# Kernel tuning notes

Measured on AMD Instinct MI355X. Metric: run time of the kernel, lower is better.

The kernel has to match this reference:

```python
import jax, jax.numpy as jnp
import numpy as np

C_FEAT = 512
HID = 256
OUT = 3
IN_DIM = C_FEAT + 2 + 2  # feat + rel_coord + rel_cell = 516


def _nearest_idx(g, size):
    # grid_sample nearest, align_corners=False: unnormalize then round (half-to-even)
    x = ((g + 1.0) * size - 1.0) / 2.0
    return jnp.clip(jnp.round(x).astype(jnp.int32), 0, size - 1)


def setup_inputs() -> dict:
    key = jax.random.key(0)
    ks = jax.random.split(key, 12)
    B, Q, H, W = 2, 65536, 48, 48
    feat = jax.random.normal(ks[0], (B, C_FEAT, H, W), dtype=jnp.float32)
    coord = jax.random.uniform(ks[1], (B, Q, 2), dtype=jnp.float32, minval=-1.0, maxval=1.0)
    cell = jnp.full((B, Q, 2), 2.0 / 256.0, dtype=jnp.float32)  # query at 256x256 output res
    def lin_init(k, fan_in, fan_out):
        s = 1.0 / np.sqrt(fan_in)
        return jax.random.uniform(k, (fan_in, fan_out), jnp.float32, -s, s)
    W0 = lin_init(ks[2], IN_DIM, HID); b0 = jnp.zeros((HID,), jnp.float32)
    W1 = lin_init(ks[3], HID, HID);    b1 = jnp.zeros((HID,), jnp.float32)
    W2 = lin_init(ks[4], HID, HID);    b2 = jnp.zeros((HID,), jnp.float32)
    W3 = lin_init(ks[5], HID, HID);    b3 = jnp.zeros((HID,), jnp.float32)
    W4 = lin_init(ks[6], HID, OUT);    b4 = jnp.zeros((OUT,), jnp.float32)
    return {"feat": feat, "coord": coord, "cell": cell,
            "W0": W0, "b0": b0, "W1": W1, "b1": b1, "W2": W2, "b2": b2,
            "W3": W3, "b3": b3, "W4": W4, "b4": b4}


def _liif(feat, coord, cell, W0, b0, W1, b1, W2, b2, W3, b3, W4, b4):
    B, C, H, W = feat.shape
    Q = coord.shape[1]
    rx = 1.0 / H  # 2 / H / 2
    ry = 1.0 / W
    eps = 1e-6
    # local ensemble shifts (vx, vy) in order [(-1,-1),(-1,1),(1,-1),(1,1)]
    shifts = jnp.array([[-1., -1.], [-1., 1.], [1., -1.], [1., 1.]], dtype=feat.dtype)
    off = shifts * jnp.array([rx, ry], dtype=feat.dtype) + eps  # [4,2]
    coord_s = jnp.clip(coord[None] + off[:, None, None, :], -1 + 1e-6, 1 - 1e-6)  # [4,B,Q,2]
    # coord[...,0] indexes H (rows), coord[...,1] indexes W (cols) [code flips before grid_sample]
    idx_r = _nearest_idx(coord_s[..., 0], H)  # [4,B,Q]
    idx_c = _nearest_idx(coord_s[..., 1], W)
    lin = idx_r * W + idx_c                   # [4,B,Q]
    flat = feat.reshape(B, C, H * W).transpose(0, 2, 1)  # [B,HW,C]
    q_feat = jnp.take_along_axis(flat[None], lin[..., None], axis=2)  # [4,B,Q,C]
    # feat_coord grid_sample == center coord of the gathered cell
    qc_r = (idx_r.astype(feat.dtype) + 0.5) * (2.0 / H) - 1.0
    qc_c = (idx_c.astype(feat.dtype) + 0.5) * (2.0 / W) - 1.0
    rel = jnp.stack([(coord[None, ..., 0] - qc_r) * H,
                     (coord[None, ..., 1] - qc_c) * W], axis=-1)  # [4,B,Q,2]
    rel_cell = cell * jnp.array([H, W], dtype=feat.dtype)          # [B,Q,2]
    rel_cell4 = jnp.broadcast_to(rel_cell[None], (4, B, Q, 2))
    inp = jnp.concatenate([q_feat, rel, rel_cell4], axis=-1)       # [4,B,Q,516]
    # shared per-point MLP
    h = jax.nn.relu(inp @ W0 + b0)
    h = jax.nn.relu(h @ W1 + b1)
    h = jax.nn.relu(h @ W2 + b2)
    h = jax.nn.relu(h @ W3 + b3)
    pred = h @ W4 + b4                                             # [4,B,Q,3]
    area = jnp.abs(rel[..., 0] * rel[..., 1]) + 1e-9               # [4,B,Q]
    tot = area.sum(axis=0)
    # swap areas 0<->3 and 1<->2 (diagonal weighting) == reverse
    w = area[::-1] / tot[None]
    return (pred * w[..., None]).sum(axis=0)                       # [B,Q,3]


def reference(feat, coord, cell, W0, b0, W1, b1, W2, b2, W3, b3, W4, b4):
    return _liif(feat, coord, cell, W0, b0, W1, b1, W2, b2, W3, b3, W4, b4)
```

## Files before the change

kernel.cpp:

```cpp
#include <hip/hip_runtime.h>
#include <hip/hip_bf16.h>
#include <math.h>

#define HH    48
#define CFEAT 512
#define HID   256
#define NPOS  (HH*HH)
#define TQ    32
#define NEV   128

typedef __attribute__((ext_vector_type(8))) short bf16x8;
typedef __attribute__((ext_vector_type(4))) float f32x4;

static __device__ __forceinline__ unsigned short f2bf(float x) {
  unsigned int u = __float_as_uint(x);
  u += 0x7fffu + ((u >> 16) & 1u);
  return (unsigned short)(u >> 16);
}

static __device__ __forceinline__ unsigned int pk2bf(float a, float b) {
  __hip_bfloat162 h2 = __float22bfloat162_rn(make_float2(a, b));
  unsigned int u; __builtin_memcpy(&u, &h2, 4); return u;
}

static __device__ __forceinline__ void rel_calc(float c0, float c1, int s,
                                                float& r0, float& r1,
                                                int& ir, int& ic) {
  float vx = (s & 2) ? 1.0f : -1.0f;
  float vy = (s & 1) ? 1.0f : -1.0f;
  const float RXY = (float)(1.0/48.0);
  const float CLO = (float)(-1.0 + 1e-6);
  const float CHI = (float)( 1.0 - 1e-6);
  float gx = __fadd_rn(c0, __fadd_rn(__fmul_rn(vx, RXY), 1e-6f));
  float gy = __fadd_rn(c1, __fadd_rn(__fmul_rn(vy, RXY), 1e-6f));
  gx = fminf(fmaxf(gx, CLO), CHI);
  gy = fminf(fmaxf(gy, CLO), CHI);
  float xr = __fmul_rn(__fsub_rn(__fmul_rn(__fadd_rn(gx, 1.0f), 48.0f), 1.0f), 0.5f);
  float xc = __fmul_rn(__fsub_rn(__fmul_rn(__fadd_rn(gy, 1.0f), 48.0f), 1.0f), 0.5f);
  ir = (int)rintf(xr); ir = ir < 0 ? 0 : (ir > HH-1 ? HH-1 : ir);
  ic = (int)rintf(xc); ic = ic < 0 ? 0 : (ic > HH-1 ? HH-1 : ic);
  const float T2 = (float)(2.0/48.0);
  float qcr = __fsub_rn(__fmul_rn(__fadd_rn((float)ir, 0.5f), T2), 1.0f);
  float qcc = __fsub_rn(__fmul_rn(__fadd_rn((float)ic, 0.5f), T2), 1.0f);
  r0 = __fmul_rn(__fsub_rn(c0, qcr), 48.0f);
  r1 = __fmul_rn(__fsub_rn(c1, qcc), 48.0f);
}

__global__ __launch_bounds__(256) void liif_precompute(
    const float* __restrict__ feat, const float* __restrict__ W0,
    const float* __restrict__ b0, float* __restrict__ P)
{
  int blk = blockIdx.x;
  int b   = blk / (NPOS/4);
  int p0  = (blk - b*(NPOS/4)) * 4;
  int n   = threadIdx.x;
  const float* f = feat + (size_t)b * CFEAT * NPOS + p0;
  float bias = b0[n];
  float a0 = bias, a1 = bias, a2 = bias, a3 = bias;
  #pragma unroll 4
  for (int c = 0; c < CFEAT; ++c) {
    float w = W0[c*HID + n];
    const float* fr = f + (size_t)c * NPOS;
    a0 += fr[0]*w; a1 += fr[1]*w; a2 += fr[2]*w; a3 += fr[3]*w;
  }
  float* Pp = P + ((size_t)b*NPOS + p0)*HID + n;
  Pp[0*HID] = a0; Pp[1*HID] = a1; Pp[2*HID] = a2; Pp[3*HID] = a3;
}

__global__ __launch_bounds__(256) void liif_convert(
    const float* __restrict__ W1, const float* __restrict__ W2,
    const float* __restrict__ W3, const float* __restrict__ W4,
    unsigned char* __restrict__ img, float* __restrict__ w4t)
{
  int blk = blockIdx.x, t = threadIdx.x;
  if (blk < 24) {
    int l = blk >> 3, kc = blk & 7;
    const float* W = (l == 0) ? W1 : (l == 1) ? W2 : W3;
    unsigned short* dst = (unsigned short*)(img + (size_t)blk * 16384);
    #pragma unroll 1
    for (int s = 0; s < 4; ++s) {
      int p    = t + s*256;
      int wc   = p >> 8;
      int nt   = (p >> 6) & 3;
      int lane = p & 63;
      int lr   = lane & 15, lk = lane >> 4;
      int n    = wc*64 + nt*16 + lr;
      int k0   = kc*32 + lk*8;
      #pragma unroll
      for (int j = 0; j < 8; ++j)
        dst[p*8 + j] = f2bf(W[(k0 + j)*256 + n]);
    }
  } else {
    for (int o = 0; o < 3; ++o) w4t[o*256 + t] = W4[t*3 + o];
  }
}


#define LDSW   65536

#define MF(A, B, C) __builtin_amdgcn_mfma_f32_16x16x32_bf16((A), (B), (C), 0, 0, 0)

#define AS1(p) ((const __attribute__((address_space(1))) void*)(unsigned long long)(const void*)(p))
#define AS3(p) ((__attribute__((address_space(3))) void*)(unsigned int)(unsigned long long)(void*)(p))

#define STAGE2(LOFF, NKC) do {                                                \
    __builtin_amdgcn_global_load_lds(                                         \
        AS1(img + (LOFF) + (NKC)*16384 + sgoff),                              \
        AS3(lds + LDSW + swoff), 16, 0, 0);                                   \
    __builtin_amdgcn_global_load_lds(                                         \
        AS1(img + (LOFF) + (NKC)*16384 + sgoff + 8192),                       \
        AS3(lds + LDSW + swoff + 8192), 16, 0, 0);                            \
  } while (0)

#define KSTEP(KC, HASN, NLOFF, NKC) do {                                      \
    const unsigned char* wb_ = lds + LDSW + lwoff;                            \
    bf16x8 w0_ = *(const bf16x8*)(wb_ + 0);                                   \
    bf16x8 w1_ = *(const bf16x8*)(wb_ + 1024);                                \
    bf16x8 w2_ = *(const bf16x8*)(wb_ + 2048);                                \
    bf16x8 w3_ = *(const bf16x8*)(wb_ + 3072);                                \
    const int ko_ = (((KC) << 6) ^ xb6);                                      \
    bf16x8 a0_ = *(const bf16x8*)(lds + rb0 + ko_);                           \
    bf16x8 a1_ = *(const bf16x8*)(lds + rb1 + ko_);                           \
    bf16x8 a2_ = *(const bf16x8*)(lds + rb2 + ko_);                           \
    bf16x8 a3_ = *(const bf16x8*)(lds + rb3 + ko_);                           \
    acc[0]  = MF(w0_, a0_, acc[0]);  acc[1]  = MF(w1_, a0_, acc[1]);          \
    acc[2]  = MF(w2_, a0_, acc[2]);  acc[3]  = MF(w3_, a0_, acc[3]);          \
    acc[4]  = MF(w0_, a1_, acc[4]);  acc[5]  = MF(w1_, a1_, acc[5]);          \
    acc[6]  = MF(w2_, a1_, acc[6]);  acc[7]  = MF(w3_, a1_, acc[7]);          \
    acc[8]  = MF(w0_, a2_, acc[8]);  acc[9]  = MF(w1_, a2_, acc[9]);          \
    acc[10] = MF(w2_, a2_, acc[10]); acc[11] = MF(w3_, a2_, acc[11]);         \
    acc[12] = MF(w0_, a3_, acc[12]); acc[13] = MF(w1_, a3_, acc[13]);         \
    acc[14] = MF(w2_, a3_, acc[14]); acc[15] = MF(w3_, a3_, acc[15]);         \
    __syncthreads();                              \
    if (HASN) { STAGE2(NLOFF, NKC); __syncthreads(); }                        \
  } while (0)

#define LAYER3(LOFF, NLOFF, LAST) do {                                        \
    _Pragma("unroll")                                                         \
    for (int i_ = 0; i_ < 16; ++i_) acc[i_] = (f32x4){0.f, 0.f, 0.f, 0.f};    \
    KSTEP(0, 1, (LOFF), 1); KSTEP(1, 1, (LOFF), 2);                           \
    KSTEP(2, 1, (LOFF), 3); KSTEP(3, 1, (LOFF), 4);                           \
    KSTEP(4, 1, (LOFF), 5); KSTEP(5, 1, (LOFF), 6);                           \
    KSTEP(6, 1, (LOFF), 7); KSTEP(7, !(LAST), (NLOFF), 0);                    \
  } while (0)

#define LAYER_WB3(BIAS) do {                                                  \
    _Pragma("unroll")                                                         \
    for (int nt_ = 0; nt_ < 4; ++nt_) {                                       \
      f32x4 bv_ = *(const f32x4*)&(BIAS)[nW + nt_*16 + lk*4];                 \
      const int cb_ = (cwb + nt_*32) ^ xwb;                                   \
      _Pragma("unroll")                                                       \
      for (int mt_ = 0; mt_ < 4; ++mt_) {                                     \
        f32x4 a_ = acc[mt_*4 + nt_];                                          \
        unsigned int lo_ = pk2bf(fmaxf(a_[0] + bv_[0], 0.f),                  \
                                 fmaxf(a_[1] + bv_[1], 0.f));                 \
        unsigned int hi_ = pk2bf(fmaxf(a_[2] + bv_[2], 0.f),                  \
                                 fmaxf(a_[3] + bv_[3], 0.f));                 \
        *(uint2*)(lds + ((m0 + mt_*16 + lr) << 9) + cb_) = make_uint2(lo_, hi_); \
      }                                                                       \
    }                                                                         \
    __syncthreads();                                                          \
  } while (0)

__global__ __launch_bounds__(512, 4)
__attribute__((amdgpu_waves_per_eu(4, 4)))
void liif_main(
    const float* __restrict__ coord, const float* __restrict__ cell,
    const float* __restrict__ P,  const float* __restrict__ W0,
    const unsigned char* __restrict__ img,
    const float* __restrict__ b1, const float* __restrict__ b2,
    const float* __restrict__ b3, const float* __restrict__ b4,
    const float* __restrict__ w4t, float* __restrict__ out)
{
  __shared__ __align__(16) unsigned char lds[81920];
  int*   lin_s = (int*)  (lds + LDSW);
  f32x4* rel4  = (f32x4*)(lds + LDSW + 512);
  float* predp = (float*)lds;

  const int t   = threadIdx.x;
  const int blk = blockIdx.x;
  const int b   = blk >> 11;
  const int q0  = (blk & 2047) * TQ;

  const int lane = t & 63;
  const int w    = t >> 6;
  const int m0   = (w >> 2) * 64;
  const int wc   = w & 3;
  const int nW   = wc * 64;
  const int lr   = lane & 15;
  const int lk   = lane >> 4;

  const size_t sgoff = (size_t)t * 16;
  const int    swoff = w * 1024;

  const int lwoff = wc*4096 + lane*16;
  const int xl  = (lr & 3) << 4;
  const int xb6 = ((lr >> 2) & 1) << 6;
  const int rb0 = ((m0 +  0 + lr) << 9) + ((lk << 4) ^ xl);
  const int rb1 = ((m0 + 16 + lr) << 9) + ((lk << 4) ^ xl);
  const int rb2 = ((m0 + 32 + lr) << 9) + ((lk << 4) ^ xl);
  const int rb3 = ((m0 + 48 + lr) << 9) + ((lk << 4) ^ xl);
  const int cwb = wc*128 + lk*8;
  const int xwb = (lr & 7) << 4;

  if (t < NEV) {
    const int e = t;
    const int q = q0 + (e >> 2);
    const int s = e & 3;
    const size_t cbase = (((size_t)b << 16) + q) * 2;
    float c0 = coord[cbase + 0];
    float c1 = coord[cbase + 1];
    float r0, r1; int ir, ic;
    rel_calc(c0, c1, s, r0, r1, ir, ic);
    lin_s[e] = ir*HH + ic;
    rel4[e] = (f32x4){r0, r1,
                      __fmul_rn(cell[cbase + 0], 48.0f),
                      __fmul_rn(cell[cbase + 1], 48.0f)};
  }
  __syncthreads();

  {
    const int cg = lane;
    const float* w0t = W0 + (size_t)512*HID + cg*4;
    f32x4 wr0 = *(const f32x4*)(w0t);
    f32x4 wr1 = *(const f32x4*)(w0t + 256);
    f32x4 wr2 = *(const f32x4*)(w0t + 512);
    f32x4 wr3 = *(const f32x4*)(w0t + 768);
    const float* Pb = P + (size_t)b * NPOS * HID + cg*4;
    const int wb = cg * 8;
    #pragma unroll 2
    for (int i = 0; i < 16; ++i) {
      const int e = w*16 + i;
      const int lin = lin_s[e];
      f32x4 rel = rel4[e];
      f32x4 pv = *(const f32x4*)(Pb + (size_t)lin*HID);
      float v0 = pv[0] + rel[0]*wr0[0] + rel[1]*wr1[0] + rel[2]*wr2[0] + rel[3]*wr3[0];
      float v1 = pv[1] + rel[0]*wr0[1] + rel[1]*wr1[1] + rel[2]*wr2[1] + rel[3]*wr3[1];
      float v2 = pv[2] + rel[0]*wr0[2] + rel[1]*wr1[2] + rel[2]*wr2[2] + rel[3]*wr3[2];
      float v3 = pv[3] + rel[0]*wr0[3] + rel[1]*wr1[3] + rel[2]*wr2[3] + rel[3]*wr3[3];
      unsigned int lo = pk2bf(fmaxf(v0, 0.f), fmaxf(v1, 0.f));
      unsigned int hi = pk2bf(fmaxf(v2, 0.f), fmaxf(v3, 0.f));
      *(uint2*)(lds + (e << 9) + (wb ^ ((e & 7) << 4))) = make_uint2(lo, hi);
    }
  }
  __syncthreads();

  STAGE2(0, 0);
  __syncthreads();

  f32x4 acc[16];
  LAYER3(0,      131072, 0);  LAYER_WB3(b1);
  LAYER3(131072, 262144, 0);  LAYER_WB3(b2);
  LAYER3(262144, 0, 1);

  {
    #pragma unroll
    for (int o = 0; o < 3; ++o) {
      float p4[4] = {0.f, 0.f, 0.f, 0.f};
      #pragma unroll
      for (int nt = 0; nt < 4; ++nt) {
        f32x4 bv = *(const f32x4*)&b3[nW + nt*16 + lk*4];
        f32x4 wv = *(const f32x4*)&w4t[o*256 + nW + nt*16 + lk*4];
        #pragma unroll
        for (int mt = 0; mt < 4; ++mt) {
          f32x4 a = acc[mt*4 + nt];
          #pragma unroll
          for (int j = 0; j < 4; ++j)
            p4[mt] += fmaxf(a[j] + bv[j], 0.f) * wv[j];
        }
      }
      #pragma unroll
      for (int mt = 0; mt < 4; ++mt) {
        float s = p4[mt];
        s += __shfl_xor(s, 16);
        s += __shfl_xor(s, 32);
        p4[mt] = s;
      }
      if (lk == 0) {
        #pragma unroll
        for (int mt = 0; mt < 4; ++mt)
          predp[wc*384 + (m0 + mt*16 + lr)*3 + o] = p4[mt];
      }
    }
  }
  __syncthreads();

  if (t < TQ*3) {
    const int q = t / 3, o = t - (t/3)*3;
    const int eb = q*4;
    const size_t cbase = (((size_t)b << 16) + (q0 + q)) * 2;
    float c0 = coord[cbase + 0];
    float c1 = coord[cbase + 1];
    float ar[4];
    #pragma unroll
    for (int s = 0; s < 4; ++s) {
      float r0, r1; int ir, ic;
      rel_calc(c0, c1, s, r0, r1, ir, ic);
      ar[s] = __fadd_rn(fabsf(__fmul_rn(r0, r1)), 1e-9f);
    }
    float pe[4];
    #pragma unroll
    for (int s = 0; s < 4; ++s) {
      const int e = eb + s;
      pe[s] = b4[o] + predp[e*3 + o] + predp[384 + e*3 + o]
                    + predp[768 + e*3 + o] + predp[1152 + e*3 + o];
    }
    float tot = ((ar[0] + ar[1]) + ar[2]) + ar[3];
    float rv = (pe[0]*ar[3] + pe[1]*ar[2] + pe[2]*ar[1] + pe[3]*ar[0]) / tot;
    out[(((size_t)b << 16) + (q0 + q))*3 + o] = rv;
  }
}

extern "C" void kernel_launch(void* const* d_in, const int* in_sizes, int n_in,
                              void* d_out, int out_size, void* d_ws, size_t ws_size,
                              hipStream_t stream)
{
  const float* feat  = (const float*)d_in[0];
  const float* coord = (const float*)d_in[1];
  const float* cell  = (const float*)d_in[2];
  const float* W0    = (const float*)d_in[3];
  const float* b0    = (const float*)d_in[4];
  const float* W1    = (const float*)d_in[5];
  const float* b1    = (const float*)d_in[6];
  const float* W2    = (const float*)d_in[7];
  const float* b2    = (const float*)d_in[8];
  const float* W3    = (const float*)d_in[9];
  const float* b3    = (const float*)d_in[10];
  const float* W4    = (const float*)d_in[11];
  const float* b4    = (const float*)d_in[12];
  float* outp = (float*)d_out;

  float*         P    = (float*)d_ws;
  unsigned char* imgp = (unsigned char*)d_ws + 4718592;
  float*         w4tp = (float*)((unsigned char*)d_ws + 4718592 + 393216);

  hipLaunchKernelGGL(liif_precompute, dim3(2*(NPOS/4)), dim3(256), 0, stream,
                     feat, W0, b0, P);
  hipLaunchKernelGGL(liif_convert, dim3(25), dim3(256), 0, stream,
                     W1, W2, W3, W4, imgp, w4tp);
  hipLaunchKernelGGL(liif_main, dim3(4096), dim3(512), 0, stream,
                     coord, cell, P, W0, imgp, b1, b2, b3, b4, w4tp, outp);
}
```

Before: 290.3 us.

## Double-buffer weight chunks and enlarge blocks to 192 rows with 12 waves

Raises queries per block from 32 to 48 (192 ensemble rows, 768 threads) so each staged weight chunk is reused by more rows. Weight staging moves to a two-buffer scheme in a larger LDS region: the next 32 KB group is prefetched while two k-steps compute on the current one, which halves the barriers per layer. Ragged tail blocks are handled by clamping and guarding query indices. The cost is more LDS per block (160 KB), which limits residency to one block per CU, plus extra guard logic.

```diff
diff --git a/kernel.cpp b/kernel.cpp
--- a/kernel.cpp
+++ b/kernel.cpp
@@ -6,8 +6,9 @@
 #define CFEAT 512
 #define HID   256
 #define NPOS  (HH*HH)
-#define TQ    32
-#define NEV   128
+#define TQ    48
+#define NEV   192
+#define NB    1366
 
 typedef __attribute__((ext_vector_type(8))) short bf16x8;
 typedef __attribute__((ext_vector_type(4))) float f32x4;
@@ -96,24 +97,29 @@
 }
 
 
-#define LDSW   65536
+#define WBASE  98304
 
 #define MF(A, B, C) __builtin_amdgcn_mfma_f32_16x16x32_bf16((A), (B), (C), 0, 0, 0)
 
 #define AS1(p) ((const __attribute__((address_space(1))) void*)(unsigned long long)(const void*)(p))
 #define AS3(p) ((__attribute__((address_space(3))) void*)(unsigned int)(unsigned long long)(void*)(p))
 
-#define STAGE2(LOFF, NKC) do {                                                \
+#define STAGEG(GOFF, BUF) do {                                                \
     __builtin_amdgcn_global_load_lds(                                         \
-        AS1(img + (LOFF) + (NKC)*16384 + sgoff),                              \
-        AS3(lds + LDSW + swoff), 16, 0, 0);                                   \
+        AS1(img + (GOFF) + sgoff),                                            \
+        AS3(lds + WBASE + (BUF)*32768 + swoff), 16, 0, 0);                    \
     __builtin_amdgcn_global_load_lds(                                         \
-        AS1(img + (LOFF) + (NKC)*16384 + sgoff + 8192),                       \
-        AS3(lds + LDSW + swoff + 8192), 16, 0, 0);                            \
-  } while (0)
-
-#define KSTEP(KC, HASN, NLOFF, NKC) do {                                      \
-    const unsigned char* wb_ = lds + LDSW + lwoff;                            \
+        AS1(img + (GOFF) + 12288 + sgoff),                                    \
+        AS3(lds + WBASE + (BUF)*32768 + 12288 + swoff), 16, 0, 0);            \
+    if (w < 8)                                                                \
+      __builtin_amdgcn_global_load_lds(                                       \
+          AS1(img + (GOFF) + 24576 + sgoff),                                  \
+          AS3(lds + WBASE + (BUF)*32768 + 24576 + swoff), 16, 0, 0);          \
+  } while (0)
+
+#define KSTEPC(KC) do {                                                       \
+    const unsigned char* wb_ = lds + WBASE + (((KC) >> 1) & 1)*32768          \
+                             + (((KC) & 1)*16384) + lwoff;                    \
     bf16x8 w0_ = *(const bf16x8*)(wb_ + 0);                                   \
     bf16x8 w1_ = *(const bf16x8*)(wb_ + 1024);                                \
     bf16x8 w2_ = *(const bf16x8*)(wb_ + 2048);                                \
@@ -131,17 +137,21 @@
     acc[10] = MF(w2_, a2_, acc[10]); acc[11] = MF(w3_, a2_, acc[11]);         \
     acc[12] = MF(w0_, a3_, acc[12]); acc[13] = MF(w1_, a3_, acc[13]);         \
     acc[14] = MF(w2_, a3_, acc[14]); acc[15] = MF(w3_, a3_, acc[15]);         \
-    __syncthreads();                              \
-    if (HASN) { STAGE2(NLOFF, NKC); __syncthreads(); }                        \
-  } while (0)
-
-#define LAYER3(LOFF, NLOFF, LAST) do {                                        \
+  } while (0)
+
+#define LGROUP(G, HASN, NGOFF) do {                                           \
+    if (HASN) STAGEG((NGOFF), (((G)+1)&1));                                   \
+    KSTEPC(2*(G)); KSTEPC(2*(G)+1);                                           \
+    __syncthreads();                                                          \
+  } while (0)
+
+#define LAYERC3(LOFF, NLOFF, LAST) do {                                       \
     _Pragma("unroll")                                                         \
     for (int i_ = 0; i_ < 16; ++i_) acc[i_] = (f32x4){0.f, 0.f, 0.f, 0.f};    \
-    KSTEP(0, 1, (LOFF), 1); KSTEP(1, 1, (LOFF), 2);                           \
-    KSTEP(2, 1, (LOFF), 3); KSTEP(3, 1, (LOFF), 4);                           \
-    KSTEP(4, 1, (LOFF), 5); KSTEP(5, 1, (LOFF), 6);                           \
-    KSTEP(6, 1, (LOFF), 7); KSTEP(7, !(LAST), (NLOFF), 0);                    \
+    LGROUP(0, 1, (LOFF) + 32768);                                             \
+    LGROUP(1, 1, (LOFF) + 65536);                                             \
+    LGROUP(2, 1, (LOFF) + 98304);                                             \
+    LGROUP(3, !(LAST), (NLOFF));                                              \
   } while (0)
 
 #define LAYER_WB3(BIAS) do {                                                  \
@@ -159,11 +169,10 @@
         *(uint2*)(lds + ((m0 + mt_*16 + lr) << 9) + cb_) = make_uint2(lo_, hi_); \
       }                                                                       \
     }                                                                         \
-    __syncthreads();                                                          \
-  } while (0)
-
-__global__ __launch_bounds__(512, 4)
-__attribute__((amdgpu_waves_per_eu(4, 4)))
+  } while (0)
+
+__global__ __launch_bounds__(768, 3)
+__attribute__((amdgpu_waves_per_eu(3, 3)))
 void liif_main(
     const float* __restrict__ coord, const float* __restrict__ cell,
     const float* __restrict__ P,  const float* __restrict__ W0,
@@ -172,15 +181,15 @@
     const float* __restrict__ b3, const float* __restrict__ b4,
     const float* __restrict__ w4t, float* __restrict__ out)
 {
-  __shared__ __align__(16) unsigned char lds[81920];
-  int*   lin_s = (int*)  (lds + LDSW);
-  f32x4* rel4  = (f32x4*)(lds + LDSW + 512);
+  __shared__ __align__(16) unsigned char lds[163840];
+  int*   lin_s = (int*)  (lds + WBASE);
+  f32x4* rel4  = (f32x4*)(lds + WBASE + 1024);
   float* predp = (float*)lds;
 
   const int t   = threadIdx.x;
   const int blk = blockIdx.x;
-  const int b   = blk >> 11;
-  const int q0  = (blk & 2047) * TQ;
+  const int b   = (blk >= NB) ? 1 : 0;
+  const int q0  = (blk - b*NB) * TQ;
 
   const int lane = t & 63;
   const int w    = t >> 6;
@@ -205,7 +214,8 @@
 
   if (t < NEV) {
     const int e = t;
-    const int q = q0 + (e >> 2);
+    int q = q0 + (e >> 2);
+    if (q > 65535) q = 65535;
     const int s = e & 3;
     const size_t cbase = (((size_t)b << 16) + q) * 2;
     float c0 = coord[cbase + 0];
@@ -245,13 +255,19 @@
   }
   __syncthreads();
 
-  STAGE2(0, 0);
+  STAGEG(0, 0);
   __syncthreads();
 
   f32x4 acc[16];
-  LAYER3(0,      131072, 0);  LAYER_WB3(b1);
-  LAYER3(131072, 262144, 0);  LAYER_WB3(b2);
-  LAYER3(262144, 0, 1);
+  LAYERC3(0, 131072, 0);
+  LAYER_WB3(b1);
+  __syncthreads();
+
+  LAYERC3(131072, 262144, 0);
+  LAYER_WB3(b2);
+  __syncthreads();
+
+  LAYERC3(262144, 0, 1);
 
   {
     #pragma unroll
@@ -279,7 +295,7 @@
       if (lk == 0) {
         #pragma unroll
         for (int mt = 0; mt < 4; ++mt)
-          predp[wc*384 + (m0 + mt*16 + lr)*3 + o] = p4[mt];
+          predp[wc*576 + (m0 + mt*16 + lr)*3 + o] = p4[mt];
       }
     }
   }
@@ -287,27 +303,30 @@
 
   if (t < TQ*3) {
     const int q = t / 3, o = t - (t/3)*3;
-    const int eb = q*4;
-    const size_t cbase = (((size_t)b << 16) + (q0 + q)) * 2;
-    float c0 = coord[cbase + 0];
-    float c1 = coord[cbase + 1];
-    float ar[4];
-    #pragma unroll
-    for (int s = 0; s < 4; ++s) {
-      float r0, r1; int ir, ic;
-      rel_calc(c0, c1, s, r0, r1, ir, ic);
-      ar[s] = __fadd_rn(fabsf(__fmul_rn(r0, r1)), 1e-9f);
+    const int qq = q0 + q;
+    if (qq < 65536) {
+      const int eb = q*4;
+      const size_t cbase = (((size_t)b << 16) + qq) * 2;
+      float c0 = coord[cbase + 0];
+      float c1 = coord[cbase + 1];
+      float ar[4];
+      #pragma unroll
+      for (int s = 0; s < 4; ++s) {
+        float r0, r1; int ir, ic;
+        rel_calc(c0, c1, s, r0, r1, ir, ic);
+        ar[s] = __fadd_rn(fabsf(__fmul_rn(r0, r1)), 1e-9f);
+      }
+      float pe[4];
+      #pragma unroll
+      for (int s = 0; s < 4; ++s) {
+        const int e = eb + s;
+        pe[s] = b4[o] + predp[e*3 + o] + predp[576 + e*3 + o]
+                      + predp[1152 + e*3 + o] + predp[1728 + e*3 + o];
+      }
+      float tot = ((ar[0] + ar[1]) + ar[2]) + ar[3];
+      float rv = (pe[0]*ar[3] + pe[1]*ar[2] + pe[2]*ar[1] + pe[3]*ar[0]) / tot;
+      out[(((size_t)b << 16) + qq)*3 + o] = rv;
     }
-    float pe[4];
-    #pragma unroll
-    for (int s = 0; s < 4; ++s) {
-      const int e = eb + s;
-      pe[s] = b4[o] + predp[e*3 + o] + predp[384 + e*3 + o]
-                    + predp[768 + e*3 + o] + predp[1152 + e*3 + o];
-    }
-    float tot = ((ar[0] + ar[1]) + ar[2]) + ar[3];
-    float rv = (pe[0]*ar[3] + pe[1]*ar[2] + pe[2]*ar[1] + pe[3]*ar[0]) / tot;
-    out[(((size_t)b << 16) + (q0 + q))*3 + o] = rv;
   }
 }
 
@@ -338,6 +357,6 @@
                      feat, W0, b0, P);
   hipLaunchKernelGGL(liif_convert, dim3(25), dim3(256), 0, stream,
                      W1, W2, W3, W4, imgp, w4tp);
-  hipLaunchKernelGGL(liif_main, dim3(4096), dim3(512), 0, stream,
+  hipLaunchKernelGGL(liif_main, dim3(2*NB), dim3(768), 0, stream,
                      coord, cell, P, W0, imgp, b1, b2, b3, b4, w4tp, outp);
 }
```

After: 291.7 us. Within noise of the previous version (+0.5%).
